# Optimization experiments

Measured on AMD Instinct MI355X. Metric: run time of the kernel, lower is better.

Reference implementation:

```python
import jax, jax.numpy as jnp
import numpy as np

N_NODES, N_EDGES, N_GRAPHS, NUM_FEATURES, NUM_CLASSES = 100000, 1600000, 512, 128, 10
EPS = 1e-5


def gat_conv(x, W, a_src, a_dst, b, src, dst, heads, out_ch):
    # PyG GATConv: h = xW -> [N,H,C]; per-node scores; leaky_relu; segment softmax over dst; scatter-add
    N = x.shape[0]
    h = (x @ W).reshape(N, heads, out_ch)
    s_src = jnp.einsum('nhc,hc->nh', h, a_src)
    s_dst = jnp.einsum('nhc,hc->nh', h, a_dst)
    score = jax.nn.leaky_relu(s_src[src] + s_dst[dst], 0.2)          # [E,H]
    m = jax.ops.segment_max(score, dst, num_segments=N)              # stable softmax per dst node
    e = jnp.exp(score - m[dst])
    denom = jax.ops.segment_sum(e, dst, num_segments=N)
    alpha = e / denom[dst]                                            # self-loops guarantee denom>0
    out = jax.ops.segment_sum(alpha[:, :, None] * h[src], dst, num_segments=N)
    return out.reshape(N, heads * out_ch) + b


def batch_norm(x, g, b):
    mu = x.mean(0)
    var = x.var(0)  # biased, as torch BN uses for normalization
    return g * (x - mu) * jax.lax.rsqrt(var + EPS) + b


def setup_inputs() -> dict:
    key = jax.random.key(0)
    ks = jax.random.split(key, 32)
    r = lambda i, shape: jax.random.normal(ks[i], shape, dtype=jnp.float32) * 0.1
    inp = {
        'x': jax.random.normal(ks[0], (N_NODES, NUM_FEATURES), dtype=jnp.float32),
        'edge_index': jax.random.randint(ks[1], (2, N_EDGES), 0, N_NODES, dtype=jnp.int64),
        'batch': jnp.sort(jax.random.randint(ks[2], (N_NODES,), 0, N_GRAPHS, dtype=jnp.int64)),
        # conv1: 128 -> 8 ch x 8 heads
        'W1': r(3, (NUM_FEATURES, 64)), 'a1s': r(4, (8, 8)), 'a1d': r(5, (8, 8)), 'b1': r(6, (64,)),
        'g1': jnp.ones(64), 'be1': jnp.zeros(64),
        'lW1': r(7, (64, 8)), 'lb1': r(8, (8,)), 'gl1': jnp.ones(8), 'bel1': jnp.zeros(8),
        # conv2: 8 -> 16 ch x 4 heads
        'W2': r(9, (8, 64)), 'a2s': r(10, (4, 16)), 'a2d': r(11, (4, 16)), 'b2': r(12, (64,)),
        'g2': jnp.ones(64), 'be2': jnp.zeros(64),
        'lW2': r(13, (64, 16)), 'lb2': r(14, (16,)), 'gl2': jnp.ones(16), 'bel2': jnp.zeros(16),
        # conv3: 16 -> 24 ch x 4 heads
        'W3': r(15, (16, 96)), 'a3s': r(16, (4, 24)), 'a3d': r(17, (4, 24)), 'b3': r(18, (96,)),
        'g3': jnp.ones(96), 'be3': jnp.zeros(96),
        'oW': r(19, (96, NUM_CLASSES)), 'ob': r(20, (NUM_CLASSES,)),
    }
    return inp


def reference(x, edge_index, batch, W1, a1s, a1d, b1, g1, be1, lW1, lb1, gl1, bel1,
              W2, a2s, a2d, b2, g2, be2, lW2, lb2, gl2, bel2,
              W3, a3s, a3d, b3, g3, be3, oW, ob):
    N = x.shape[0]
    loops = jnp.arange(N, dtype=edge_index.dtype)
    src = jnp.concatenate([edge_index[0], loops])  # PyG add_self_loops default
    dst = jnp.concatenate([edge_index[1], loops])

    h = gat_conv(x, W1, a1s, a1d, b1, src, dst, 8, 8)
    h = jax.nn.relu(batch_norm(h, g1, be1))
    h = jax.nn.relu(batch_norm(h @ lW1 + lb1, gl1, bel1))

    h = gat_conv(h, W2, a2s, a2d, b2, src, dst, 4, 16)
    h = jax.nn.relu(batch_norm(h, g2, be2))
    h = jax.nn.relu(batch_norm(h @ lW2 + lb2, gl2, bel2))

    h = gat_conv(h, W3, a3s, a3d, b3, src, dst, 4, 24)
    h = jax.nn.relu(batch_norm(h, g3, be3))

    sums = jax.ops.segment_sum(h, batch, num_segments=N_GRAPHS)
    cnts = jax.ops.segment_sum(jnp.ones((N,), h.dtype), batch, num_segments=N_GRAPHS)
    pooled = sums / jnp.maximum(cnts, 1.0)[:, None]
    return pooled @ oW + ob
```

## Files before the change

### kernel.cpp

```cpp
#include <hip/hip_runtime.h>
#include <hip/hip_fp16.h>
#include <math.h>

#define NN 100000
#define NE 1600000
#define ET (NE + NN)
#define NG 512
#define STATS_BLOCKS 240
#define SCAN_B 1024
#define SCAN_NB ((NN + SCAN_B - 1) / SCAN_B)
#define PSLOTS (ET + 7 * NN + 16)

#define BSH 9
#define NB  ((NN + 511) / 512)
#define BCAP 12288
#define CHUNK 4096


__global__ __launch_bounds__(256) void part_pass1(const int* __restrict__ ei,
                                                  int* __restrict__ bcur,
                                                  unsigned* __restrict__ pairs) {
    __shared__ unsigned pck[CHUNK];
    __shared__ unsigned ordv[CHUNK];
    __shared__ unsigned char bkt[CHUNK];
    __shared__ unsigned char obkt[CHUNK];
    __shared__ int hist[NB + 1];
    __shared__ int lofs[NB + 1];
    __shared__ int cur[NB + 1];
    __shared__ int gpos[NB];
    __shared__ int lh[256];

    int t = threadIdx.x;
    int base = blockIdx.x * CHUNK;
    for (int i = t; i <= NB; i += 256) hist[i] = 0;
    __syncthreads();
    for (int i = t; i < CHUNK; i += 256) {
        int e = base + i;
        int b;
        unsigned p = 0;
        if (e < ET) {
            int s, d;
            if (e < NE) { s = ei[e]; d = ei[NE + e]; }
            else        { s = d = e - NE; }
            b = d >> BSH;
            p = ((unsigned)s << BSH) | (unsigned)(d & 511);
        } else b = NB;
        bkt[i] = (unsigned char)b;
        pck[i] = p;
        atomicAdd(&hist[b], 1);
    }
    __syncthreads();
    int v = (t <= NB) ? hist[t] : 0;
    lh[t] = v;
    __syncthreads();
    for (int off = 1; off < 256; off <<= 1) {
        int x = (t >= off) ? lh[t - off] : 0;
        __syncthreads();
        lh[t] += x;
        __syncthreads();
    }
    if (t <= NB) { lofs[t] = lh[t] - v; cur[t] = lh[t] - v; }
    __syncthreads();
    if (t < NB) {
        int h = hist[t];
        gpos[t] = (h > 0) ? atomicAdd(&bcur[t], h) : 0;
    }
    __syncthreads();
    for (int i = t; i < CHUNK; i += 256) {
        int b = bkt[i];
        int pos = atomicAdd(&cur[b], 1);
        ordv[pos] = pck[i];
        obkt[pos] = (unsigned char)b;
    }
    __syncthreads();
    int nvalid = lofs[NB];
    for (int i = t; i < nvalid; i += 256) {
        int b = obkt[i];
        int dst = gpos[b] + (i - lofs[b]);
        if (dst < BCAP) pairs[(size_t)b * BCAP + dst] = ordv[i];
    }
}


__global__ __launch_bounds__(256) void bucket_counts(const unsigned* __restrict__ pairs,
                                                     const int* __restrict__ bcur,
                                                     int* __restrict__ counts) {
    __shared__ int lhist[512];
    int b = blockIdx.x;
    int t = threadIdx.x;
    for (int i = t; i < 512; i += 256) lhist[i] = 0;
    __syncthreads();
    int cnt = min(bcur[b], BCAP);
    const unsigned* seg = pairs + (size_t)b * BCAP;
    for (int i = t; i < cnt; i += 256)
        atomicAdd(&lhist[seg[i] & 511], 1);
    __syncthreads();
    int nbase = b << BSH;
    for (int i = t; i < 512; i += 256) {
        int n = nbase + i;
        if (n < NN) counts[n] = lhist[i];
    }
}


__global__ __launch_bounds__(256) void bucket_scatter(const unsigned* __restrict__ pairs,
                                                      const int* __restrict__ bcur,
                                                      const int* __restrict__ offsets,
                                                      int* __restrict__ srcs) {
    __shared__ int cur[512];
    int b = blockIdx.x;
    int t = threadIdx.x;
    int nbase = b << BSH;
    for (int i = t; i < 512; i += 256) {
        int n = nbase + i;
        cur[i] = (n < NN) ? offsets[n] : 0;
    }
    __syncthreads();
    int cnt = min(bcur[b], BCAP);
    const unsigned* seg = pairs + (size_t)b * BCAP;
    for (int i = t; i < cnt; i += 256) {
        unsigned p = seg[i];
        int pos = atomicAdd(&cur[p & 511], 1);
        srcs[pos] = (int)(p >> BSH);
    }
}


__global__ void graph_bounds(const int* __restrict__ batch, int* __restrict__ goff) {
    int g = blockIdx.x * blockDim.x + threadIdx.x;
    if (g > NG) return;
    int lo = 0, hi = NN;
    while (lo < hi) {
        int mid = (lo + hi) >> 1;
        if (batch[mid] < g) lo = mid + 1; else hi = mid;
    }
    goff[g] = lo;
}


__global__ void scan_reduce(const int* __restrict__ in, int* __restrict__ bsum) {
    __shared__ int lds[256];
    int b = blockIdx.x, t = threadIdx.x;
    int s = 0;
    for (int i = t; i < SCAN_B; i += 256) {
        int idx = b * SCAN_B + i;
        if (idx < NN) s += (in[idx] + 7) & ~7;
    }
    lds[t] = s;
    __syncthreads();
    for (int off = 128; off > 0; off >>= 1) {
        if (t < off) lds[t] += lds[t + off];
        __syncthreads();
    }
    if (t == 0) bsum[b] = lds[0];
}

__global__ void scan_bsums(const int* __restrict__ bsum, int nb, int* __restrict__ boff,
                           int* __restrict__ total_loc) {
    __shared__ int lds[128];
    int t = threadIdx.x;
    int v = (t < nb) ? bsum[t] : 0;
    lds[t] = v;
    __syncthreads();
    for (int off = 1; off < 128; off <<= 1) {
        int x = (t >= off) ? lds[t - off] : 0;
        __syncthreads();
        lds[t] += x;
        __syncthreads();
    }
    if (t < nb) boff[t] = lds[t] - v;
    if (t == nb - 1) {
        boff[nb] = lds[t];
        if (total_loc) *total_loc = lds[t];
    }
}

__global__ void scan_final(const int* __restrict__ in, const int* __restrict__ boff,
                           int* __restrict__ out) {
    __shared__ int lds[SCAN_B];
    int b = blockIdx.x, t = threadIdx.x;
    int idx = b * SCAN_B + t;
    int v = (idx < NN) ? ((in[idx] + 7) & ~7) : 0;
    lds[t] = v;
    __syncthreads();
    for (int off = 1; off < SCAN_B; off <<= 1) {
        int x = (t >= off) ? lds[t - off] : 0;
        __syncthreads();
        lds[t] += x;
        __syncthreads();
    }
    if (idx < NN) out[idx] = boff[b] + lds[t] - v;
}


__global__ __launch_bounds__(256) void gemm1(const float* __restrict__ X,
                                             const float* __restrict__ W,
                                             const float* __restrict__ a_s,
                                             const float* __restrict__ a_d,
                                             __half* __restrict__ Hh,
                                             float* __restrict__ SS,
                                             float* __restrict__ SD) {
    __shared__ float wl[128 * 64];
    __shared__ float xl[32 * 132];
    int t = threadIdx.x;
    int n0 = blockIdx.x * 32;
    for (int i = t * 4; i < 128 * 64; i += 1024)
        *(float4*)&wl[i] = *(const float4*)&W[i];
    for (int i = t * 4; i < 32 * 128; i += 1024) {
        int r = i >> 7, c = i & 127;
        int n = n0 + r;
        float4 v = (n < NN) ? *(const float4*)&X[(size_t)n * 128 + c] : make_float4(0, 0, 0, 0);
        *(float4*)&xl[r * 132 + c] = v;
    }
    __syncthreads();
    int cg = (t & 15) * 4;
    int ng = (t >> 4) * 2;
    float acc[2][4] = {};
    for (int k = 0; k < 128; ++k) {
        float4 w4 = *(float4*)&wl[k * 64 + cg];
        #pragma unroll
        for (int j = 0; j < 2; ++j) {
            float xv = xl[(ng + j) * 132 + k];
            acc[j][0] += xv * w4.x; acc[j][1] += xv * w4.y;
            acc[j][2] += xv * w4.z; acc[j][3] += xv * w4.w;
        }
    }
    int hd = cg >> 3;
    int half = cg & 7;
    #pragma unroll
    for (int j = 0; j < 2; ++j) {
        int n = n0 + ng + j;
        float p1 = 0.f, p2 = 0.f;
        #pragma unroll
        for (int k = 0; k < 4; ++k) {
            p1 += acc[j][k] * a_s[hd * 8 + half + k];
            p2 += acc[j][k] * a_d[hd * 8 + half + k];
        }
        float f1 = p1 + __shfl_xor(p1, 1, 64);
        float f2 = p2 + __shfl_xor(p2, 1, 64);
        if (n < NN) {
            __half2 q0 = __floats2half2_rn(acc[j][0], acc[j][1]);
            __half2 q1 = __floats2half2_rn(acc[j][2], acc[j][3]);
            *(__half2*)&Hh[(size_t)n * 64 + cg] = q0;
            *(__half2*)&Hh[(size_t)n * 64 + cg + 2] = q1;
            if (half == 0) {
                SS[(unsigned)n * 8 + hd] = f1;
                SD[(unsigned)n * 8 + hd] = f2;
            }
        }
    }
}


template <int HEADS, int C, int PL, int GRP>
__global__ __launch_bounds__(256) void gat_kernel(const __half* __restrict__ Hh,
                                                  const float* __restrict__ SS,
                                                  const float* __restrict__ SD,
                                                  const int* __restrict__ offsets,
                                                  const int* __restrict__ counts,
                                                  const int* __restrict__ srcs,
                                                  const float* __restrict__ bias,
                                                  __half* __restrict__ GO) {
    constexpr int CH = HEADS * C;
    constexpr int LG = (GRP == 16) ? 4 : 3;
    int wid = blockIdx.x * (blockDim.x >> 6) + (threadIdx.x >> 6);
    int lane = threadIdx.x & 63;
    if (wid >= NN) return;
    int ch0 = lane * PL;
    bool active = ch0 < CH;
    int ch0l = active ? ch0 : 0;
    int head = active ? (ch0 / C) : 0;
    int headGRP = head * GRP;
    int beg = offsets[wid], end = offsets[wid + 1];
    int deg = counts[wid];
    int sEdge = lane & (GRP - 1);
    int sHead = (lane >> LG) & (HEADS - 1);
    float sdvS = SD[(unsigned)wid * HEADS + sHead];
    float s = 0.f, a0 = 0.f, a1 = 0.f;
    for (int e = beg; e < end; e += GRP) {
        int myIdx = e + sEdge;
        int mySrc = srcs[myIdx];
        float sc = SS[(unsigned)mySrc * HEADS + sHead] + sdvS;
        sc = fmaxf(sc, 0.f) + 0.2f * fminf(sc, 0.f);
        float myW = (myIdx - beg) < deg ? __expf(sc) : 0.f;
        int sv[GRP];
        float wv[GRP];
        #pragma unroll
        for (int i = 0; i < GRP; ++i) {
            sv[i] = __shfl(mySrc, headGRP + i, 64);
            wv[i] = __shfl(myW, headGRP + i, 64);
        }
        if (PL == 1) {
            float hv[GRP];
            #pragma unroll
            for (int i = 0; i < GRP; ++i)
                hv[i] = __half2float(Hh[(unsigned)(sv[i] * CH) + ch0l]);
            float pw[GRP / 2], pa[GRP / 2];
            #pragma unroll
            for (int i = 0; i < GRP / 2; ++i) {
                pw[i] = wv[2 * i] + wv[2 * i + 1];
                pa[i] = wv[2 * i] * hv[2 * i] + wv[2 * i + 1] * hv[2 * i + 1];
            }
            #pragma unroll
            for (int st = GRP / 4; st >= 1; st >>= 1) {
                #pragma unroll
                for (int i = 0; i < st; ++i) { pw[i] += pw[i + st]; pa[i] += pa[i + st]; }
            }
            s += pw[0];
            a0 += pa[0];
        } else {
            float hv0[GRP], hv1[GRP];
            #pragma unroll
            for (int i = 0; i < GRP; ++i) {
                __half2 hp = *(const __half2*)&Hh[(unsigned)(sv[i] * CH) + ch0l];
                hv0[i] = __low2float(hp); hv1[i] = __high2float(hp);
            }
            float pw[GRP / 2], pa[GRP / 2], pb[GRP / 2];
            #pragma unroll
            for (int i = 0; i < GRP / 2; ++i) {
                pw[i] = wv[2 * i] + wv[2 * i + 1];
                pa[i] = wv[2 * i] * hv0[2 * i] + wv[2 * i + 1] * hv0[2 * i + 1];
                pb[i] = wv[2 * i] * hv1[2 * i] + wv[2 * i + 1] * hv1[2 * i + 1];
            }
            #pragma unroll
            for (int st = GRP / 4; st >= 1; st >>= 1) {
                #pragma unroll
                for (int i = 0; i < st; ++i) { pw[i] += pw[i + st]; pa[i] += pa[i + st]; pb[i] += pb[i + st]; }
            }
            s += pw[0];
            a0 += pa[0];
            a1 += pb[0];
        }
    }
    if (active) {
        float inv = 1.f / s;
        if (PL == 2) {
            *(__half2*)&GO[(unsigned)(wid * CH) + ch0] =
                __floats2half2_rn(a0 * inv + bias[ch0], a1 * inv + bias[ch0 + 1]);
        } else {
            GO[(unsigned)(wid * CH) + ch0] = __float2half(a0 * inv + bias[ch0]);
        }
    }
}


__global__ void stats_kernel(const float* __restrict__ X, int Nn, int C,
                             float* __restrict__ partial) {
    int t = threadIdx.x;
    int c = t % C;
    int grp = t / C;
    int G_ = blockDim.x / C;
    float s = 0.f, q = 0.f;
    for (int n = blockIdx.x * G_ + grp; n < Nn; n += gridDim.x * G_) {
        float v = X[(size_t)n * C + c];
        s += v; q += v * v;
    }
    extern __shared__ float lds[];
    lds[t] = s; lds[blockDim.x + t] = q;
    __syncthreads();
    for (int off = blockDim.x >> 1; off >= C; off >>= 1) {
        if (t < off) {
            lds[t] += lds[t + off];
            lds[blockDim.x + t] += lds[blockDim.x + t + off];
        }
        __syncthreads();
    }
    if (t < C) {
        partial[(size_t)blockIdx.x * 2 * C + t] = lds[t];
        partial[(size_t)blockIdx.x * 2 * C + C + t] = lds[blockDim.x + t];
    }
}

__global__ void stats_h_kernel(const __half* __restrict__ X, int Nn, int C,
                               float* __restrict__ partial) {
    int t = threadIdx.x;
    int c = t % C;
    int grp = t / C;
    int G_ = blockDim.x / C;
    float s = 0.f, q = 0.f;
    for (int n = blockIdx.x * G_ + grp; n < Nn; n += gridDim.x * G_) {
        float v = __half2float(X[(size_t)n * C + c]);
        s += v; q += v * v;
    }
    extern __shared__ float lds[];
    lds[t] = s; lds[blockDim.x + t] = q;
    __syncthreads();
    for (int off = blockDim.x >> 1; off >= C; off >>= 1) {
        if (t < off) {
            lds[t] += lds[t + off];
            lds[blockDim.x + t] += lds[blockDim.x + t + off];
        }
        __syncthreads();
    }
    if (t < C) {
        partial[(size_t)blockIdx.x * 2 * C + t] = lds[t];
        partial[(size_t)blockIdx.x * 2 * C + C + t] = lds[blockDim.x + t];
    }
}

__global__ void bn_finalize(const float* __restrict__ partial, int nb, int C, float invN,
                            const float* __restrict__ g, const float* __restrict__ be,
                            float* __restrict__ scale, float* __restrict__ shift) {
    extern __shared__ float red[];
    int t = threadIdx.x;
    int c = t % C;
    int grp = t / C;
    int G_ = blockDim.x / C;
    float s = 0.f, q = 0.f;
    for (int b = grp; b < nb; b += G_) {
        s += partial[(size_t)b * 2 * C + c];
        q += partial[(size_t)b * 2 * C + C + c];
    }
    red[t] = s; red[blockDim.x + t] = q;
    __syncthreads();
    for (int off = blockDim.x >> 1; off >= C; off >>= 1) {
        if (t < off) {
            red[t] += red[t + off];
            red[blockDim.x + t] += red[blockDim.x + t + off];
        }
        __syncthreads();
    }
    if (t < C) {
        float mean = red[t] * invN;
        float var = fmaxf(red[blockDim.x + t] * invN - mean * mean, 0.f);
        float rs = rsqrtf(var + 1e-5f);
        float sc = g[t] * rs;
        scale[t] = sc;
        shift[t] = be[t] - mean * sc;
    }
}


template <int KOUT>
__global__ __launch_bounds__(256) void bnrelu_linear(const __half* __restrict__ X,
                                                     const float* __restrict__ scale,
                                                     const float* __restrict__ shift,
                                                     const float* __restrict__ Lw,
                                                     const float* __restrict__ lb,
                                                     float* __restrict__ U) {
    __shared__ float tl[64 * 65];
    int t = threadIdx.x;
    int n0 = blockIdx.x * 64;
    for (int i = t * 4; i < 64 * 64; i += 1024) {
        int r = i >> 6, cc = i & 63;
        int n = n0 + r;
        float vv[4] = {0.f, 0.f, 0.f, 0.f};
        if (n < NN) {
            float2 v0 = __half22float2(*(const __half2*)&X[(size_t)n * 64 + cc]);
            float2 v1 = __half22float2(*(const __half2*)&X[(size_t)n * 64 + cc + 2]);
            vv[0] = v0.x; vv[1] = v0.y; vv[2] = v1.x; vv[3] = v1.y;
        }
        #pragma unroll
        for (int j = 0; j < 4; ++j)
            tl[r * 65 + cc + j] = fmaxf(vv[j] * scale[cc + j] + shift[cc + j], 0.f);
    }
    __syncthreads();
    int nl = t & 63;
    int kg = (t >> 6) * (KOUT / 4);
    float acc[KOUT / 4] = {};
    for (int l = 0; l < 64; ++l) {
        float v = tl[nl * 65 + l];
        #pragma unroll
        for (int j = 0; j < KOUT / 4; ++j) acc[j] += v * Lw[l * KOUT + kg + j];
    }
    int n = n0 + nl;
    if (n < NN)
        #pragma unroll
        for (int j = 0; j < KOUT / 4; ++j)
            U[(size_t)n * KOUT + kg + j] = acc[j] + lb[kg + j];
}


template <int CIN, int COUT, int H, int C>
__global__ __launch_bounds__(256) void bnrelu_gemm(const float* __restrict__ U,
                                                   const float* __restrict__ scale,
                                                   const float* __restrict__ shift,
                                                   const float* __restrict__ W,
                                                   const float* __restrict__ a_s,
                                                   const float* __restrict__ a_d,
                                                   __half* __restrict__ Hh,
                                                   float* __restrict__ SS,
                                                   float* __restrict__ SD) {
    static_assert(COUT / 4 == C && H == 4, "thread-per-head mapping");
    int t = threadIdx.x;
    int nl = t >> 2;
    int q = t & 3;
    int n = blockIdx.x * 64 + nl;
    if (n >= NN) return;
    constexpr int CPT = COUT / 4;
    float v[CIN];
    #pragma unroll
    for (int c = 0; c < CIN; ++c)
        v[c] = fmaxf(U[(size_t)n * CIN + c] * scale[c] + shift[c], 0.f);
    float acc[CPT] = {};
    #pragma unroll
    for (int c = 0; c < CIN; ++c) {
        #pragma unroll
        for (int j = 0; j < CPT; ++j) acc[j] += v[c] * W[c * COUT + q * CPT + j];
    }
    float s1 = 0.f, s2 = 0.f;
    #pragma unroll
    for (int j = 0; j < CPT; ++j) {
        s1 += acc[j] * a_s[q * C + j];
        s2 += acc[j] * a_d[q * C + j];
    }
    SS[(unsigned)n * H + q] = s1;
    SD[(unsigned)n * H + q] = s2;
    #pragma unroll
    for (int j = 0; j < CPT; j += 2)
        *(__half2*)&Hh[(size_t)n * COUT + q * CPT + j] = __floats2half2_rn(acc[j], acc[j + 1]);
}


__global__ __launch_bounds__(256) void pool_kernel(const __half* __restrict__ GO,
                                                   const float* __restrict__ scale,
                                                   const float* __restrict__ shift,
                                                   const int* __restrict__ goff,
                                                   float* __restrict__ pooled) {
    __shared__ float red[8][32];
    int g = blockIdx.x;
    int ch = blockIdx.y * 32 + (threadIdx.x & 31);
    int row = threadIdx.x >> 5;
    int beg = goff[g], end = goff[g + 1];
    float sc = scale[ch], sh = shift[ch];
    float s = 0.f;
    for (int n = beg + row; n < end; n += 8)
        s += fmaxf(__half2float(GO[(size_t)n * 96 + ch]) * sc + sh, 0.f);
    red[row][threadIdx.x & 31] = s;
    __syncthreads();
    if (row == 0) {
        #pragma unroll
        for (int r = 1; r < 8; ++r) s += red[r][threadIdx.x & 31];
        float cnt = (float)(end - beg);
        pooled[g * 96 + ch] = s / fmaxf(cnt, 1.f);
    }
}

__global__ void final_gemm(const float* __restrict__ pooled, const float* __restrict__ oW,
                           const float* __restrict__ ob, float* __restrict__ out) {
    int idx = blockIdx.x * blockDim.x + threadIdx.x;
    if (idx >= NG * 10) return;
    int g = idx / 10, k = idx % 10;
    float s = ob[k];
    for (int c = 0; c < 96; ++c) s += pooled[g * 96 + c] * oW[c * 10 + k];
    out[idx] = s;
}


extern "C" void kernel_launch(void* const* d_in, const int* in_sizes, int n_in,
                              void* d_out, int out_size, void* d_ws, size_t ws_size,
                              hipStream_t stream) {
    const float* x   = (const float*)d_in[0];
    const int*   ei  = (const int*)d_in[1];
    const int*   bat = (const int*)d_in[2];
    const float *W1 = (const float*)d_in[3], *a1s = (const float*)d_in[4],
                *a1d = (const float*)d_in[5], *b1 = (const float*)d_in[6],
                *g1 = (const float*)d_in[7], *be1 = (const float*)d_in[8],
                *lW1 = (const float*)d_in[9], *lb1 = (const float*)d_in[10],
                *gl1 = (const float*)d_in[11], *bel1 = (const float*)d_in[12],
                *W2 = (const float*)d_in[13], *a2s = (const float*)d_in[14],
                *a2d = (const float*)d_in[15], *b2 = (const float*)d_in[16],
                *g2 = (const float*)d_in[17], *be2 = (const float*)d_in[18],
                *lW2 = (const float*)d_in[19], *lb2 = (const float*)d_in[20],
                *gl2 = (const float*)d_in[21], *bel2 = (const float*)d_in[22],
                *W3 = (const float*)d_in[23], *a3s = (const float*)d_in[24],
                *a3d = (const float*)d_in[25], *b3 = (const float*)d_in[26],
                *g3 = (const float*)d_in[27], *be3 = (const float*)d_in[28],
                *oW = (const float*)d_in[29], *ob = (const float*)d_in[30];
    float* out = (float*)d_out;

    int* iw      = (int*)d_ws;
    int* bcur    = iw;
    int* counts  = bcur + NB;
    int* offsets = counts + NN;
    int* goff    = offsets + NN + 1;
    int* bsum    = goff + NG + 1;
    int* boff    = bsum + SCAN_NB;
    int* srcs    = boff + SCAN_NB + 1;
    float* fw      = (float*)(srcs + PSLOTS);
    __half* GOh    = (__half*)fw;
    float* Ub      = fw + (size_t)NN * 96;
    float* SSb     = Ub + (size_t)NN * 16;
    float* SDb     = SSb + (size_t)NN * 8;
    float* partial = SDb + (size_t)NN * 8;
    float* scaleA  = partial + STATS_BLOCKS * 192;
    float* shiftA  = scaleA + 96;
    float* scaleB  = shiftA + 96;
    float* shiftB  = scaleB + 16;
    float* pooled  = shiftB + 16;
    __half* Hh     = (__half*)(pooled + NG * 96);
    unsigned* pairs = (unsigned*)GOh;

    const float invN = 1.0f / (float)NN;

    hipMemsetAsync(bcur, 0, NB * sizeof(int), stream);
    hipMemsetAsync(srcs, 0, (size_t)PSLOTS * sizeof(int), stream);
    part_pass1<<<(ET + CHUNK - 1) / CHUNK, 256, 0, stream>>>(ei, bcur, pairs);
    graph_bounds<<<3, 256, 0, stream>>>(bat, goff);
    bucket_counts<<<NB, 256, 0, stream>>>(pairs, bcur, counts);
    scan_reduce<<<SCAN_NB, 256, 0, stream>>>(counts, bsum);
    scan_bsums<<<1, 128, 0, stream>>>(bsum, SCAN_NB, boff, &offsets[NN]);
    scan_final<<<SCAN_NB, SCAN_B, 0, stream>>>(counts, boff, offsets);
    bucket_scatter<<<NB, 256, 0, stream>>>(pairs, bcur, offsets, srcs);

    gemm1<<<(NN + 31) / 32, 256, 0, stream>>>(x, W1, a1s, a1d, Hh, SSb, SDb);
    gat_kernel<8, 8, 1, 8><<<(NN + 3) / 4, 256, 0, stream>>>(Hh, SSb, SDb, offsets, counts, srcs, b1, GOh);
    stats_h_kernel<<<STATS_BLOCKS, 256, 2 * 256 * sizeof(float), stream>>>(GOh, NN, 64, partial);
    bn_finalize<<<1, 512, 2 * 512 * sizeof(float), stream>>>(partial, STATS_BLOCKS, 64, invN, g1, be1, scaleA, shiftA);
    bnrelu_linear<8><<<(NN + 63) / 64, 256, 0, stream>>>(GOh, scaleA, shiftA, lW1, lb1, Ub);
    stats_kernel<<<STATS_BLOCKS, 256, 2 * 256 * sizeof(float), stream>>>(Ub, NN, 8, partial);
    bn_finalize<<<1, 512, 2 * 512 * sizeof(float), stream>>>(partial, STATS_BLOCKS, 8, invN, gl1, bel1, scaleB, shiftB);

    bnrelu_gemm<8, 64, 4, 16><<<(NN + 63) / 64, 256, 0, stream>>>(Ub, scaleB, shiftB, W2, a2s, a2d, Hh, SSb, SDb);
    gat_kernel<4, 16, 1, 16><<<(NN + 3) / 4, 256, 0, stream>>>(Hh, SSb, SDb, offsets, counts, srcs, b2, GOh);
    stats_h_kernel<<<STATS_BLOCKS, 256, 2 * 256 * sizeof(float), stream>>>(GOh, NN, 64, partial);
    bn_finalize<<<1, 512, 2 * 512 * sizeof(float), stream>>>(partial, STATS_BLOCKS, 64, invN, g2, be2, scaleA, shiftA);
    bnrelu_linear<16><<<(NN + 63) / 64, 256, 0, stream>>>(GOh, scaleA, shiftA, lW2, lb2, Ub);
    stats_kernel<<<STATS_BLOCKS, 256, 2 * 256 * sizeof(float), stream>>>(Ub, NN, 16, partial);
    bn_finalize<<<1, 512, 2 * 512 * sizeof(float), stream>>>(partial, STATS_BLOCKS, 16, invN, gl2, bel2, scaleB, shiftB);

    bnrelu_gemm<16, 96, 4, 24><<<(NN + 63) / 64, 256, 0, stream>>>(Ub, scaleB, shiftB, W3, a3s, a3d, Hh, SSb, SDb);
    gat_kernel<4, 24, 2, 8><<<(NN + 3) / 4, 256, 0, stream>>>(Hh, SSb, SDb, offsets, counts, srcs, b3, GOh);
    stats_h_kernel<<<STATS_BLOCKS, 192, 2 * 192 * sizeof(float), stream>>>(GOh, NN, 96, partial);
    bn_finalize<<<1, 768, 2 * 768 * sizeof(float), stream>>>(partial, STATS_BLOCKS, 96, invN, g3, be3, scaleA, shiftA);

    pool_kernel<<<dim3(NG, 3), 256, 0, stream>>>(GOh, scaleA, shiftA, goff, pooled);
    final_gemm<<<(NG * 10 + 255) / 256, 256, 0, stream>>>(pooled, oW, ob, out);
}
```

Measured before the change: 610.6 us.

## Fuse BN stats into bnrelu_linear and software-pipeline GAT edge score loads

The separate stats_kernel pass over the linear output is removed. bnrelu_linear now reduces per-block sum and sum-of-squares with wave shuffles and writes partials, and bn_finalize reduces over the 1563 blocks. The GAT edge loop also prefetches the next group's src index and source score while the current group is aggregated, to hide gather latency. The trade-off is a larger partial buffer and a bigger finalize reduction, and the prefetch reads one group past the end, which PSLOTS padding now covers.

```diff
diff --git a/kernel.cpp b/kernel.cpp
--- a/kernel.cpp
+++ b/kernel.cpp
@@ -9,7 +9,8 @@
 #define STATS_BLOCKS 240
 #define SCAN_B 1024
 #define SCAN_NB ((NN + SCAN_B - 1) / SCAN_B)
-#define PSLOTS (ET + 7 * NN + 16)
+#define PSLOTS (ET + 7 * NN + 32)
+#define NLBLK ((NN + 63) / 64)
 
 #define BSH 9
 #define NB  ((NN + 511) / 512)
@@ -276,13 +277,25 @@
     int sEdge = lane & (GRP - 1);
     int sHead = (lane >> LG) & (HEADS - 1);
     float sdvS = SD[(unsigned)wid * HEADS + sHead];
+    int myIdx = beg + sEdge;
+    int mySrc = srcs[myIdx];
+    {
+        float sc = SS[(unsigned)mySrc * HEADS + sHead] + sdvS;
+        sc = fmaxf(sc, 0.f) + 0.2f * fminf(sc, 0.f);
+        mySrc = mySrc;
+        myIdx = myIdx;
+    }
+    float myW;
+    {
+        float sc = SS[(unsigned)mySrc * HEADS + sHead] + sdvS;
+        sc = fmaxf(sc, 0.f) + 0.2f * fminf(sc, 0.f);
+        myW = (myIdx - beg) < deg ? __expf(sc) : 0.f;
+    }
     float s = 0.f, a0 = 0.f, a1 = 0.f;
     for (int e = beg; e < end; e += GRP) {
-        int myIdx = e + sEdge;
-        int mySrc = srcs[myIdx];
-        float sc = SS[(unsigned)mySrc * HEADS + sHead] + sdvS;
-        sc = fmaxf(sc, 0.f) + 0.2f * fminf(sc, 0.f);
-        float myW = (myIdx - beg) < deg ? __expf(sc) : 0.f;
+        int nIdx = e + GRP + sEdge;
+        int nSrc = srcs[nIdx];
+        float nSS = SS[(unsigned)nSrc * HEADS + sHead];
         int sv[GRP];
         float wv[GRP];
         #pragma unroll
@@ -331,6 +344,10 @@
             a0 += pa[0];
             a1 += pb[0];
         }
+        float sc = nSS + sdvS;
+        sc = fmaxf(sc, 0.f) + 0.2f * fminf(sc, 0.f);
+        myW = (nIdx - beg) < deg ? __expf(sc) : 0.f;
+        mySrc = nSrc;
     }
     if (active) {
         float inv = 1.f / s;
@@ -344,33 +361,6 @@
 }
 
 
-__global__ void stats_kernel(const float* __restrict__ X, int Nn, int C,
-                             float* __restrict__ partial) {
-    int t = threadIdx.x;
-    int c = t % C;
-    int grp = t / C;
-    int G_ = blockDim.x / C;
-    float s = 0.f, q = 0.f;
-    for (int n = blockIdx.x * G_ + grp; n < Nn; n += gridDim.x * G_) {
-        float v = X[(size_t)n * C + c];
-        s += v; q += v * v;
-    }
-    extern __shared__ float lds[];
-    lds[t] = s; lds[blockDim.x + t] = q;
-    __syncthreads();
-    for (int off = blockDim.x >> 1; off >= C; off >>= 1) {
-        if (t < off) {
-            lds[t] += lds[t + off];
-            lds[blockDim.x + t] += lds[blockDim.x + t + off];
-        }
-        __syncthreads();
-    }
-    if (t < C) {
-        partial[(size_t)blockIdx.x * 2 * C + t] = lds[t];
-        partial[(size_t)blockIdx.x * 2 * C + C + t] = lds[blockDim.x + t];
-    }
-}
-
 __global__ void stats_h_kernel(const __half* __restrict__ X, int Nn, int C,
                                float* __restrict__ partial) {
     int t = threadIdx.x;
@@ -437,7 +427,8 @@
                                                      const float* __restrict__ shift,
                                                      const float* __restrict__ Lw,
                                                      const float* __restrict__ lb,
-                                                     float* __restrict__ U) {
+                                                     float* __restrict__ U,
+                                                     float* __restrict__ partial) {
     __shared__ float tl[64 * 65];
     int t = threadIdx.x;
     int n0 = blockIdx.x * 64;
@@ -464,10 +455,27 @@
         for (int j = 0; j < KOUT / 4; ++j) acc[j] += v * Lw[l * KOUT + kg + j];
     }
     int n = n0 + nl;
+    float uval[KOUT / 4];
+    #pragma unroll
+    for (int j = 0; j < KOUT / 4; ++j)
+        uval[j] = (n < NN) ? acc[j] + lb[kg + j] : 0.f;
     if (n < NN)
         #pragma unroll
         for (int j = 0; j < KOUT / 4; ++j)
-            U[(size_t)n * KOUT + kg + j] = acc[j] + lb[kg + j];
+            U[(size_t)n * KOUT + kg + j] = uval[j];
+    #pragma unroll
+    for (int j = 0; j < KOUT / 4; ++j) {
+        float sm = uval[j], sq = uval[j] * uval[j];
+        #pragma unroll
+        for (int off = 32; off >= 1; off >>= 1) {
+            sm += __shfl_xor(sm, off, 64);
+            sq += __shfl_xor(sq, off, 64);
+        }
+        if (nl == 0) {
+            partial[(size_t)blockIdx.x * 2 * KOUT + kg + j] = sm;
+            partial[(size_t)blockIdx.x * 2 * KOUT + KOUT + kg + j] = sq;
+        }
+    }
 }
 
 
@@ -583,7 +591,7 @@
     float* SSb     = Ub + (size_t)NN * 16;
     float* SDb     = SSb + (size_t)NN * 8;
     float* partial = SDb + (size_t)NN * 8;
-    float* scaleA  = partial + STATS_BLOCKS * 192;
+    float* scaleA  = partial + 51200;
     float* shiftA  = scaleA + 96;
     float* scaleB  = shiftA + 96;
     float* shiftB  = scaleB + 16;
@@ -607,17 +615,15 @@
     gat_kernel<8, 8, 1, 8><<<(NN + 3) / 4, 256, 0, stream>>>(Hh, SSb, SDb, offsets, counts, srcs, b1, GOh);
     stats_h_kernel<<<STATS_BLOCKS, 256, 2 * 256 * sizeof(float), stream>>>(GOh, NN, 64, partial);
     bn_finalize<<<1, 512, 2 * 512 * sizeof(float), stream>>>(partial, STATS_BLOCKS, 64, invN, g1, be1, scaleA, shiftA);
-    bnrelu_linear<8><<<(NN + 63) / 64, 256, 0, stream>>>(GOh, scaleA, shiftA, lW1, lb1, Ub);
-    stats_kernel<<<STATS_BLOCKS, 256, 2 * 256 * sizeof(float), stream>>>(Ub, NN, 8, partial);
-    bn_finalize<<<1, 512, 2 * 512 * sizeof(float), stream>>>(partial, STATS_BLOCKS, 8, invN, gl1, bel1, scaleB, shiftB);
+    bnrelu_linear<8><<<NLBLK, 256, 0, stream>>>(GOh, scaleA, shiftA, lW1, lb1, Ub, partial);
+    bn_finalize<<<1, 512, 2 * 512 * sizeof(float), stream>>>(partial, NLBLK, 8, invN, gl1, bel1, scaleB, shiftB);
 
     bnrelu_gemm<8, 64, 4, 16><<<(NN + 63) / 64, 256, 0, stream>>>(Ub, scaleB, shiftB, W2, a2s, a2d, Hh, SSb, SDb);
     gat_kernel<4, 16, 1, 16><<<(NN + 3) / 4, 256, 0, stream>>>(Hh, SSb, SDb, offsets, counts, srcs, b2, GOh);
     stats_h_kernel<<<STATS_BLOCKS, 256, 2 * 256 * sizeof(float), stream>>>(GOh, NN, 64, partial);
     bn_finalize<<<1, 512, 2 * 512 * sizeof(float), stream>>>(partial, STATS_BLOCKS, 64, invN, g2, be2, scaleA, shiftA);
-    bnrelu_linear<16><<<(NN + 63) / 64, 256, 0, stream>>>(GOh, scaleA, shiftA, lW2, lb2, Ub);
-    stats_kernel<<<STATS_BLOCKS, 256, 2 * 256 * sizeof(float), stream>>>(Ub, NN, 16, partial);
-    bn_finalize<<<1, 512, 2 * 512 * sizeof(float), stream>>>(partial, STATS_BLOCKS, 16, invN, gl2, bel2, scaleB, shiftB);
+    bnrelu_linear<16><<<NLBLK, 256, 0, stream>>>(GOh, scaleA, shiftA, lW2, lb2, Ub, partial);
+    bn_finalize<<<1, 512, 2 * 512 * sizeof(float), stream>>>(partial, NLBLK, 16, invN, gl2, bel2, scaleB, shiftB);
 
     bnrelu_gemm<16, 96, 4, 24><<<(NN + 63) / 64, 256, 0, stream>>>(Ub, scaleB, shiftB, W3, a3s, a3d, Hh, SSb, SDb);
     gat_kernel<4, 24, 2, 8><<<(NN + 3) / 4, 256, 0, stream>>>(Hh, SSb, SDb, offsets, counts, srcs, b3, GOh);
```

Result: slower. 640.6 us (+4.9%).
